# Kernel tuning notes

Hardware: AMD Instinct MI355X
Metric: run time of the kernel (lower is better)

The kernel has to match this reference:

```python
import jax, jax.numpy as jnp
import numpy as np

H = 16   # num_attention_heads
G = 4    # num_gqa_groups
D = 64   # head_dim = hidden // H
HIDDEN = 1024
KV_DIM = HIDDEN // H * G  # 256
EPS = 1e-5


def setup_inputs() -> dict:
    key = jax.random.key(0)
    k0, k1, k2, k3 = jax.random.split(key, 4)
    x = jax.random.normal(k0, (8, 4096, HIDDEN), dtype=jnp.float32)
    query_weight = jax.random.normal(k1, (HIDDEN, HIDDEN), dtype=jnp.float32) * 0.02
    key_weight = jax.random.normal(k2, (KV_DIM, HIDDEN), dtype=jnp.float32) * 0.02
    value_weight = jax.random.normal(k3, (KV_DIM, HIDDEN), dtype=jnp.float32) * 0.02
    return {
        "x": x,
        "query_weight": query_weight,
        "key_weight": key_weight,
        "value_weight": value_weight,
        "query_bias": jnp.zeros((HIDDEN,), jnp.float32),
        "key_bias": jnp.zeros((KV_DIM,), jnp.float32),
        "value_bias": jnp.zeros((KV_DIM,), jnp.float32),
        "layer_norm_weight": jnp.ones((HIDDEN,), jnp.float32),
        "layer_norm_bias": jnp.zeros((HIDDEN,), jnp.float32),
    }


def reference(x, query_weight, key_weight, value_weight, query_bias, key_bias,
              value_bias, layer_norm_weight, layer_norm_bias):
    b, s, _ = x.shape
    # Shared LayerNorm (q is k is v path in apply_qkv_norm)
    mu = jnp.mean(x, axis=-1, keepdims=True)
    var = jnp.mean(jnp.square(x - mu), axis=-1, keepdims=True)
    xn = (x - mu) * jax.lax.rsqrt(var + EPS) * layer_norm_weight + layer_norm_bias
    # Q/K/V projections (F.linear: x @ W.T + b)
    q = xn @ query_weight.T + query_bias           # [b, s, H*D]
    k = xn @ key_weight.T + key_bias               # [b, s, G*1*D]
    v = xn @ value_weight.T + value_bias           # [b, s, G*1*D]
    # 'b s (h d) -> b h s d'
    q = q.reshape(b, s, H, D).transpose(0, 2, 1, 3)           # [b, H, s, D]
    # 'b s (g h d) -> b h (g s) d' with h = KV_DIM//(G*D) = 1
    def kv_rearrange(t):
        t = t.reshape(b, s, G, 1, D)                          # b s g h d
        t = t.transpose(0, 3, 2, 1, 4)                        # b h g s d
        return t.reshape(b, 1, G * s, D)                      # [b, 1, G*s, D]
    return q, kv_rearrange(k), kv_rearrange(v)
```

## Files before the change

kernel.cpp:

```cpp
#include <hip/hip_runtime.h>
#include <hip/hip_bf16.h>


#define HIDDEN 1024
#define NTOK   32768
#define BM     128
#define BN     128
#define BK     64

typedef __bf16 bf16x8 __attribute__((ext_vector_type(8)));
typedef float  f32x4  __attribute__((ext_vector_type(4)));

#define GLOBAL_AS(p) ((const __attribute__((address_space(1))) void*)(p))
#define LDS_AS(p)    ((__attribute__((address_space(3))) void*)(p))

__device__ __forceinline__ unsigned short f2bf(float f) {
  union { float f; unsigned int i; } x; x.f = f;
  unsigned int r = x.i + 0x7FFFu + ((x.i >> 16) & 1u);
  return (unsigned short)(r >> 16);
}

__global__ __launch_bounds__(256) void ln_kernel(
    const float* __restrict__ x,
    const float* __restrict__ gamma,
    const float* __restrict__ beta,
    unsigned short* __restrict__ xn) {
  const int row = blockIdx.x;
  const int t   = threadIdx.x;
  const size_t base = (size_t)row * HIDDEN;

  const float4 v = ((const float4*)(x + base))[t];
  float s  = v.x + v.y + v.z + v.w;
  float s2 = v.x*v.x + v.y*v.y + v.z*v.z + v.w*v.w;
#pragma unroll
  for (int off = 32; off >= 1; off >>= 1) {
    s  += __shfl_xor(s,  off);
    s2 += __shfl_xor(s2, off);
  }
  __shared__ float red[8];
  const int w = t >> 6;
  if ((t & 63) == 0) { red[w] = s; red[4 + w] = s2; }
  __syncthreads();
  s  = red[0] + red[1] + red[2] + red[3];
  s2 = red[4] + red[5] + red[6] + red[7];
  const float mu   = s * (1.0f / HIDDEN);
  const float rstd = rsqrtf(s2 * (1.0f / HIDDEN) - mu * mu + 1e-5f);

  const float4 g  = ((const float4*)gamma)[t];
  const float4 bb = ((const float4*)beta)[t];
  ushort4 o;
  o.x = f2bf((v.x - mu) * rstd * g.x + bb.x);
  o.y = f2bf((v.y - mu) * rstd * g.y + bb.y);
  o.z = f2bf((v.z - mu) * rstd * g.z + bb.z);
  o.w = f2bf((v.w - mu) * rstd * g.w + bb.w);
  ((ushort4*)(xn + base))[t] = o;
}

__global__ __launch_bounds__(256) void cvt_kernel(
    const float* __restrict__ src, unsigned short* __restrict__ dst) {
  const int i = blockIdx.x * 256 + threadIdx.x;
  const float4 v = ((const float4*)src)[i];
  ushort4 o;
  o.x = f2bf(v.x); o.y = f2bf(v.y); o.z = f2bf(v.z); o.w = f2bf(v.w);
  ((ushort4*)dst)[i] = o;
}

__global__ __launch_bounds__(256) void qkv_gemm(
    const unsigned short* __restrict__ xn,
    const unsigned short* __restrict__ wq,
    const unsigned short* __restrict__ wk,
    const unsigned short* __restrict__ wv,
    const float* __restrict__ bq,
    const float* __restrict__ bk,
    const float* __restrict__ bv,
    float* __restrict__ out) {
  __shared__ unsigned short Alds[BM * BK];
  __shared__ unsigned short Blds[BN * BK];

  const int tn   = blockIdx.x;
  const int brow = blockIdx.y * BM;

  const unsigned short* wptr; const float* biasptr;
  int segcol; size_t obase; int hg;
  if (tn < 8)       { wptr = wq; biasptr = bq; segcol = tn * BN;        obase = 0u;        hg = 16; }
  else if (tn < 10) { wptr = wk; biasptr = bk; segcol = (tn - 8) * BN;  obase = 33554432u; hg = 4;  }
  else              { wptr = wv; biasptr = bv; segcol = (tn - 10) * BN; obase = 41943040u; hg = 4;  }

  const int t = threadIdx.x;
  const int w = t >> 6, lane = t & 63;
  const int wr = (w >> 1) * 64;
  const int wc = (w & 1)  * 64;

  f32x4 acc[4][4];
#pragma unroll
  for (int m = 0; m < 4; ++m)
#pragma unroll
    for (int n = 0; n < 4; ++n) acc[m][n] = (f32x4){0.f, 0.f, 0.f, 0.f};

  const int srow = t >> 3;
  const int scol = (t & 7) * 8;
  const unsigned short* aSrc = xn   + (size_t)(brow   + srow) * HIDDEN + scol;
  const unsigned short* bSrc = wptr + (size_t)(segcol + srow) * HIDDEN + scol;
  const int ldsWave = (w << 6) * 8;

  for (int kt = 0; kt < HIDDEN; kt += BK) {
#pragma unroll
    for (int i = 0; i < 4; ++i) {
      __builtin_amdgcn_global_load_lds(GLOBAL_AS(aSrc + (size_t)i * 32 * HIDDEN + kt),
                                       LDS_AS(Alds + i * 2048 + ldsWave), 16, 0, 0);
      __builtin_amdgcn_global_load_lds(GLOBAL_AS(bSrc + (size_t)i * 32 * HIDDEN + kt),
                                       LDS_AS(Blds + i * 2048 + ldsWave), 16, 0, 0);
    }
    __syncthreads();

    bf16x8 af[2][4], bfr[2][4];
#pragma unroll
    for (int kk = 0; kk < 2; ++kk) {
#pragma unroll
      for (int m = 0; m < 4; ++m)
        af[kk][m]  = *(const bf16x8*)(Alds + (wr + m * 16 + (lane & 15)) * BK + kk * 32 + (lane >> 4) * 8);
#pragma unroll
      for (int n = 0; n < 4; ++n)
        bfr[kk][n] = *(const bf16x8*)(Blds + (wc + n * 16 + (lane & 15)) * BK + kk * 32 + (lane >> 4) * 8);
    }
#pragma unroll
    for (int m = 0; m < 4; ++m)
#pragma unroll
      for (int n = 0; n < 4; ++n) {
        acc[m][n] = __builtin_amdgcn_mfma_f32_16x16x32_bf16(af[0][m], bfr[0][n], acc[m][n], 0, 0, 0);
        acc[m][n] = __builtin_amdgcn_mfma_f32_16x16x32_bf16(af[1][m], bfr[1][n], acc[m][n], 0, 0, 0);
      }
    __syncthreads();
  }

  const int col_l = lane & 15;
  const int row_l = (lane >> 4) * 4;
#pragma unroll
  for (int n = 0; n < 4; ++n) {
    const int ncol = segcol + wc + n * 16 + col_l;
    const float bias = biasptr[ncol];
    const int g = ncol >> 6;
    const int d = ncol & 63;
#pragma unroll
    for (int m = 0; m < 4; ++m) {
#pragma unroll
      for (int j = 0; j < 4; ++j) {
        const int token = brow + wr + m * 16 + row_l + j;
        const int b = token >> 12, s = token & 4095;
        const size_t off = obase + (size_t)(b * hg + g) * 262144u + (size_t)s * 64u + d;
        out[off] = acc[m][n][j] + bias;
      }
    }
  }
}

extern "C" void kernel_launch(void* const* d_in, const int* in_sizes, int n_in,
                              void* d_out, int out_size, void* d_ws, size_t ws_size,
                              hipStream_t stream) {
  const float* x  = (const float*)d_in[0];
  const float* wq = (const float*)d_in[1];
  const float* wk = (const float*)d_in[2];
  const float* wv = (const float*)d_in[3];
  const float* bq = (const float*)d_in[4];
  const float* bk = (const float*)d_in[5];
  const float* bv = (const float*)d_in[6];
  const float* g  = (const float*)d_in[7];
  const float* be = (const float*)d_in[8];
  float* out = (float*)d_out;

  unsigned short* xn  = (unsigned short*)d_ws;
  unsigned short* wqb = (unsigned short*)((char*)d_ws + (64u << 20));
  unsigned short* wkb = wqb + 1024 * 1024;
  unsigned short* wvb = wkb + 256 * 1024;

  ln_kernel<<<NTOK, 256, 0, stream>>>(x, g, be, xn);
  cvt_kernel<<<1024, 256, 0, stream>>>(wq, wqb);
  cvt_kernel<<<256,  256, 0, stream>>>(wk, wkb);
  cvt_kernel<<<256,  256, 0, stream>>>(wv, wvb);
  dim3 grid(12, 256);
  qkv_gemm<<<grid, 256, 0, stream>>>(xn, wqb, wkb, wvb, bq, bk, bv, out);
}
```

Measured before the change: 207.8 us.

## Rewrite QKV GEMM with 256x256 tiles, 4-stage LDS pipeline and swizzled LDS

The GEMM now uses 256x256 output tiles with 512 threads (8 waves, each computing 128x64) and BK=32. A 4-buffer LDS ring is prefetched three steps ahead with global_load_lds and partial vmcnt waits, so loads overlap MFMA work. LDS columns are XOR-swizzled to reduce bank conflicts, and the block index is remapped for L2 locality. In exchange it needs 128KB of LDS per block and many more accumulator registers, which may limit occupancy.

```diff
diff --git a/kernel.cpp b/kernel.cpp
--- a/kernel.cpp
+++ b/kernel.cpp
@@ -4,9 +4,6 @@
 
 #define HIDDEN 1024
 #define NTOK   32768
-#define BM     128
-#define BN     128
-#define BK     64
 
 typedef __bf16 bf16x8 __attribute__((ext_vector_type(8)));
 typedef float  f32x4  __attribute__((ext_vector_type(4)));
@@ -65,7 +62,7 @@
   ((ushort4*)dst)[i] = o;
 }
 
-__global__ __launch_bounds__(256) void qkv_gemm(
+__global__ __launch_bounds__(512, 2) void qkv_gemm(
     const unsigned short* __restrict__ xn,
     const unsigned short* __restrict__ wq,
     const unsigned short* __restrict__ wk,
@@ -74,78 +71,99 @@
     const float* __restrict__ bk,
     const float* __restrict__ bv,
     float* __restrict__ out) {
-  __shared__ unsigned short Alds[BM * BK];
-  __shared__ unsigned short Blds[BN * BK];
+  __shared__ unsigned short Al[4 * 8192];
+  __shared__ unsigned short Bl[4 * 8192];
 
-  const int tn   = blockIdx.x;
-  const int brow = blockIdx.y * BM;
+  const int bid = blockIdx.x;
+  const int swz = (bid & 7) * 96 + (bid >> 3);
+  const int mt  = swz / 6;
+  const int nt  = swz % 6;
+  const int brow = mt * 256;
 
-  const unsigned short* wptr; const float* biasptr;
+  const unsigned short* wbase; const float* biasptr;
   int segcol; size_t obase; int hg;
-  if (tn < 8)       { wptr = wq; biasptr = bq; segcol = tn * BN;        obase = 0u;        hg = 16; }
-  else if (tn < 10) { wptr = wk; biasptr = bk; segcol = (tn - 8) * BN;  obase = 33554432u; hg = 4;  }
-  else              { wptr = wv; biasptr = bv; segcol = (tn - 10) * BN; obase = 41943040u; hg = 4;  }
+  if (nt < 4)       { wbase = wq + (size_t)nt * 256 * HIDDEN; biasptr = bq; segcol = nt * 256; obase = 0u;        hg = 16; }
+  else if (nt == 4) { wbase = wk;                             biasptr = bk; segcol = 0;        obase = 33554432u; hg = 4;  }
+  else              { wbase = wv;                             biasptr = bv; segcol = 0;        obase = 41943040u; hg = 4;  }
 
   const int t = threadIdx.x;
   const int w = t >> 6, lane = t & 63;
-  const int wr = (w >> 1) * 64;
-  const int wc = (w & 1)  * 64;
+  const int wm = w >> 2, wn = w & 3;
+  const int l15 = lane & 15, hi = lane >> 4;
 
-  f32x4 acc[4][4];
+  const int r0 = t >> 2,        c0 = ((t & 3) * 8) ^ (((r0 >> 1) & 3) << 3);
+  const int r1 = (512 + t) >> 2, c1 = ((t & 3) * 8) ^ (((r1 >> 1) & 3) << 3);
+  const unsigned short* aS0 = xn    + (size_t)(brow + r0) * HIDDEN + c0;
+  const unsigned short* aS1 = xn    + (size_t)(brow + r1) * HIDDEN + c1;
+  const unsigned short* bS0 = wbase + (size_t)r0 * HIDDEN + c0;
+  const unsigned short* bS1 = wbase + (size_t)r1 * HIDDEN + c1;
+  const int ldsW = w * 512;
+
+  const int sz   = ((l15 >> 1) & 3) << 3;
+  const int aOff0 = (wm * 128 + l15) * 32 + ((hi * 8) ^ sz);
+  const int bOff0 = (wn * 64  + l15) * 32 + ((hi * 8) ^ sz);
+
+  f32x4 acc[8][4];
 #pragma unroll
-  for (int m = 0; m < 4; ++m)
+  for (int m = 0; m < 8; ++m)
 #pragma unroll
     for (int n = 0; n < 4; ++n) acc[m][n] = (f32x4){0.f, 0.f, 0.f, 0.f};
 
-  const int srow = t >> 3;
-  const int scol = (t & 7) * 8;
-  const unsigned short* aSrc = xn   + (size_t)(brow   + srow) * HIDDEN + scol;
-  const unsigned short* bSrc = wptr + (size_t)(segcol + srow) * HIDDEN + scol;
-  const int ldsWave = (w << 6) * 8;
+  auto stage = [&](int j) {
+    const int bb = (j & 3) * 8192;
+    const int kk = j << 5;
+    __builtin_amdgcn_global_load_lds(GLOBAL_AS(aS0 + kk), LDS_AS(Al + bb + ldsW),        16, 0, 0);
+    __builtin_amdgcn_global_load_lds(GLOBAL_AS(aS1 + kk), LDS_AS(Al + bb + 4096 + ldsW), 16, 0, 0);
+    __builtin_amdgcn_global_load_lds(GLOBAL_AS(bS0 + kk), LDS_AS(Bl + bb + ldsW),        16, 0, 0);
+    __builtin_amdgcn_global_load_lds(GLOBAL_AS(bS1 + kk), LDS_AS(Bl + bb + 4096 + ldsW), 16, 0, 0);
+  };
 
-  for (int kt = 0; kt < HIDDEN; kt += BK) {
+  auto compute = [&](int j) {
+    const unsigned short* Ab = Al + (j & 3) * 8192;
+    const unsigned short* Bb = Bl + (j & 3) * 8192;
+    bf16x8 bfr[4];
 #pragma unroll
-    for (int i = 0; i < 4; ++i) {
-      __builtin_amdgcn_global_load_lds(GLOBAL_AS(aSrc + (size_t)i * 32 * HIDDEN + kt),
-                                       LDS_AS(Alds + i * 2048 + ldsWave), 16, 0, 0);
-      __builtin_amdgcn_global_load_lds(GLOBAL_AS(bSrc + (size_t)i * 32 * HIDDEN + kt),
-                                       LDS_AS(Blds + i * 2048 + ldsWave), 16, 0, 0);
-    }
-    __syncthreads();
-
-    bf16x8 af[2][4], bfr[2][4];
+    for (int n = 0; n < 4; ++n) bfr[n] = *(const bf16x8*)(Bb + bOff0 + n * 512);
+    bf16x8 af[8];
 #pragma unroll
-    for (int kk = 0; kk < 2; ++kk) {
+    for (int m = 0; m < 8; ++m) af[m] = *(const bf16x8*)(Ab + aOff0 + m * 512);
+    __builtin_amdgcn_s_setprio(1);
 #pragma unroll
-      for (int m = 0; m < 4; ++m)
-        af[kk][m]  = *(const bf16x8*)(Alds + (wr + m * 16 + (lane & 15)) * BK + kk * 32 + (lane >> 4) * 8);
+    for (int m = 0; m < 8; ++m)
 #pragma unroll
       for (int n = 0; n < 4; ++n)
-        bfr[kk][n] = *(const bf16x8*)(Blds + (wc + n * 16 + (lane & 15)) * BK + kk * 32 + (lane >> 4) * 8);
-    }
-#pragma unroll
-    for (int m = 0; m < 4; ++m)
-#pragma unroll
-      for (int n = 0; n < 4; ++n) {
-        acc[m][n] = __builtin_amdgcn_mfma_f32_16x16x32_bf16(af[0][m], bfr[0][n], acc[m][n], 0, 0, 0);
-        acc[m][n] = __builtin_amdgcn_mfma_f32_16x16x32_bf16(af[1][m], bfr[1][n], acc[m][n], 0, 0, 0);
-      }
-    __syncthreads();
-  }
+        acc[m][n] = __builtin_amdgcn_mfma_f32_16x16x32_bf16(af[m], bfr[n], acc[m][n], 0, 0, 0);
+    __builtin_amdgcn_s_setprio(0);
+  };
 
-  const int col_l = lane & 15;
-  const int row_l = (lane >> 4) * 4;
+#define KSTEP(J, VMN, PF) do {                                        \
+    asm volatile("s_waitcnt vmcnt(" #VMN ")" ::: "memory");           \
+    __builtin_amdgcn_s_barrier();                                     \
+    __builtin_amdgcn_sched_barrier(0);                                \
+    if (PF) stage((J) + 3);                                           \
+    compute(J);                                                       \
+  } while (0)
+
+  stage(0); stage(1); stage(2);
+  for (int j = 0; j < 29; ++j) { KSTEP(j, 8, true); }
+  KSTEP(29, 8, false);
+  KSTEP(30, 4, false);
+  KSTEP(31, 0, false);
+#undef KSTEP
+
+  const int col_l = l15;
+  const int row_l = hi * 4;
 #pragma unroll
   for (int n = 0; n < 4; ++n) {
-    const int ncol = segcol + wc + n * 16 + col_l;
-    const float bias = biasptr[ncol];
-    const int g = ncol >> 6;
-    const int d = ncol & 63;
+    const int ncolseg = segcol + wn * 64 + n * 16 + col_l;
+    const float bias = biasptr[ncolseg];
+    const int g = ncolseg >> 6;
+    const int d = ncolseg & 63;
 #pragma unroll
-    for (int m = 0; m < 4; ++m) {
+    for (int m = 0; m < 8; ++m) {
 #pragma unroll
       for (int j = 0; j < 4; ++j) {
-        const int token = brow + wr + m * 16 + row_l + j;
+        const int token = brow + wm * 128 + m * 16 + row_l + j;
         const int b = token >> 12, s = token & 4095;
         const size_t off = obase + (size_t)(b * hg + g) * 262144u + (size_t)s * 64u + d;
         out[off] = acc[m][n][j] + bias;
@@ -177,6 +195,5 @@
   cvt_kernel<<<1024, 256, 0, stream>>>(wq, wqb);
   cvt_kernel<<<256,  256, 0, stream>>>(wk, wkb);
   cvt_kernel<<<256,  256, 0, stream>>>(wv, wvb);
-  dim3 grid(12, 256);
-  qkv_gemm<<<grid, 256, 0, stream>>>(xn, wqb, wkb, wvb, bq, bk, bv, out);
+  qkv_gemm<<<768, 512, 0, stream>>>(xn, wqb, wkb, wvb, bq, bk, bv, out);
 }
```

Result: faster. 198.9 us (-4.3%).
